# Performance work log

Measured on AMD Instinct MI355X. Metric: run time of the kernel, lower is better.

## Reference

```python
import jax, jax.numpy as jnp
import numpy as np

B, H, S, D = 2, 16, 1024, 64

def setup_inputs() -> dict:
    key = jax.random.key(0)
    k1, k2 = jax.random.split(key)
    # x1 is the output of a softmax (attention probabilities): non-negative, rows sum to 1
    logits = jax.random.normal(k1, (B, H, S, S), dtype=jnp.float32)
    x1 = jax.nn.softmax(logits, axis=-1)
    x2 = jax.random.normal(k2, (B, H, S, D), dtype=jnp.float32)
    return {"x1": x1, "x2": x2}

def reference(x1, x2):
    # Forward of EfficientMemoryGEMMWithSoftmax: exact batched GEMM.
    # (The outlier/low-bit compression only affects what is cached for backward;
    #  the forward output is the exact product.)
    return jnp.einsum('bhsk,bhkd->bhsd', x1, x2)
```

## Files before the change

kernel.cpp:

```cpp
#include <hip/hip_runtime.h>
#include <hip/hip_bf16.h>

typedef __attribute__((ext_vector_type(8))) short short8_t;
typedef __attribute__((ext_vector_type(4))) short short4_t;
typedef __attribute__((ext_vector_type(4))) float f32x4;

#define S_DIM   1024
#define D_DIM   64
#define BM      128
#define KC      64
#define NCHUNK  (S_DIM / KC)
#define BSTRIDE 72
#define THREADS 512

__device__ __forceinline__ ushort f2bf(float f) {
    __hip_bfloat16 h = __float2bfloat16(f);
    return __builtin_bit_cast(ushort, h);
}

__global__ __launch_bounds__(THREADS, 1)
void gemm_sm_kernel(const float* __restrict__ x1,
                    const float* __restrict__ x2,
                    float* __restrict__ out) {
    __shared__ ushort lds_a[BM * KC];
    __shared__ ushort lds_b[D_DIM * BSTRIDE];

    const int tid = threadIdx.x;
    const int bid = blockIdx.x;
    const int batch   = (bid & 7) * 4 + (bid >> 6);
    const int rowtile = (bid >> 3) & 7;
    const int row0    = rowtile * BM;

    const float* Abase = x1 + (size_t)batch * (S_DIM * S_DIM) + (size_t)row0 * S_DIM;
    const float* Bbase = x2 + (size_t)batch * (S_DIM * D_DIM);
    float*       Cbase = out + (size_t)batch * (S_DIM * D_DIM) + (size_t)row0 * D_DIM;

    const int w = tid >> 6;
    const int l = tid & 63;

    const int ar  = tid >> 2;
    const int akq = tid & 3;
    const float* aptr = Abase + (size_t)ar * S_DIM + akq * 16;
    const int aw_swz  = (ar & 7) << 3;
    const int aw_base = ar * KC + akq * 16;
    const int aw0 = (aw_base    ) ^ aw_swz;
    const int aw1 = (aw_base + 8) ^ aw_swz;

    const int bd  = l;
    const int bk0 = w * 4;

    const int wm = w >> 1, wn = w & 1;
    const int fr = l & 15, fg = l >> 4;
    int aidx[2][2], bidx[2][2];
    #pragma unroll
    for (int mf = 0; mf < 2; ++mf) {
        const int row = wm * 32 + mf * 16 + fr;
        #pragma unroll
        for (int ks = 0; ks < 2; ++ks)
            aidx[mf][ks] = (row * KC + ks * 32 + fg * 8) ^ ((row & 7) << 3);
    }
    #pragma unroll
    for (int nf = 0; nf < 2; ++nf) {
        const int col = wn * 32 + nf * 16 + fr;
        #pragma unroll
        for (int ks = 0; ks < 2; ++ks)
            bidx[nf][ks] = col * BSTRIDE + ks * 32 + fg * 8;
    }

    float areg[16];
    float breg[8];

    auto load_chunk = [&](int t) {
        const float* p = aptr + t * KC;
        #pragma unroll
        for (int i = 0; i < 4; ++i) {
            float4 v = *reinterpret_cast<const float4*>(p + i * 4);
            areg[i * 4 + 0] = v.x; areg[i * 4 + 1] = v.y;
            areg[i * 4 + 2] = v.z; areg[i * 4 + 3] = v.w;
        }
        const float* bp = Bbase + (size_t)t * KC * D_DIM + bd;
        #pragma unroll
        for (int i = 0; i < 2; ++i)
            #pragma unroll
            for (int j = 0; j < 4; ++j)
                breg[i * 4 + j] = bp[(bk0 + 32 * i + j) * D_DIM];
    };

    auto store_lds = [&]() {
        short8_t v0, v1;
        #pragma unroll
        for (int j = 0; j < 8; ++j) v0[j] = (short)f2bf(areg[j]);
        #pragma unroll
        for (int j = 0; j < 8; ++j) v1[j] = (short)f2bf(areg[8 + j]);
        *reinterpret_cast<short8_t*>(&lds_a[aw0]) = v0;
        *reinterpret_cast<short8_t*>(&lds_a[aw1]) = v1;
        #pragma unroll
        for (int i = 0; i < 2; ++i) {
            short4_t bv;
            #pragma unroll
            for (int j = 0; j < 4; ++j) bv[j] = (short)f2bf(breg[i * 4 + j]);
            *reinterpret_cast<short4_t*>(&lds_b[bd * BSTRIDE + bk0 + 32 * i]) = bv;
        }
    };

    f32x4 acc[2][2];
    #pragma unroll
    for (int mf = 0; mf < 2; ++mf)
        #pragma unroll
        for (int nf = 0; nf < 2; ++nf)
            acc[mf][nf] = f32x4{0.f, 0.f, 0.f, 0.f};

    load_chunk(0);

    for (int t = 0; t < NCHUNK; ++t) {
        __syncthreads();
        store_lds();
        __syncthreads();
        if (t + 1 < NCHUNK) load_chunk(t + 1);

        short8_t af[2][2], bf[2][2];
        #pragma unroll
        for (int mf = 0; mf < 2; ++mf)
            #pragma unroll
            for (int ks = 0; ks < 2; ++ks)
                af[mf][ks] = *reinterpret_cast<const short8_t*>(&lds_a[aidx[mf][ks]]);
        #pragma unroll
        for (int nf = 0; nf < 2; ++nf)
            #pragma unroll
            for (int ks = 0; ks < 2; ++ks)
                bf[nf][ks] = *reinterpret_cast<const short8_t*>(&lds_b[bidx[nf][ks]]);

        #pragma unroll
        for (int ks = 0; ks < 2; ++ks)
            #pragma unroll
            for (int mf = 0; mf < 2; ++mf)
                #pragma unroll
                for (int nf = 0; nf < 2; ++nf)
                    acc[mf][nf] = __builtin_amdgcn_mfma_f32_16x16x32_bf16(
                        af[mf][ks], bf[nf][ks], acc[mf][nf], 0, 0, 0);
    }

    #pragma unroll
    for (int mf = 0; mf < 2; ++mf)
        #pragma unroll
        for (int nf = 0; nf < 2; ++nf)
            #pragma unroll
            for (int j = 0; j < 4; ++j) {
                const int r = wm * 32 + mf * 16 + fg * 4 + j;
                const int c = wn * 32 + nf * 16 + fr;
                Cbase[(size_t)r * D_DIM + c] = acc[mf][nf][j];
            }
}

extern "C" void kernel_launch(void* const* d_in, const int* in_sizes, int n_in,
                              void* d_out, int out_size, void* d_ws, size_t ws_size,
                              hipStream_t stream) {
    const float* x1 = (const float*)d_in[0];
    const float* x2 = (const float*)d_in[1];
    float* out = (float*)d_out;
    dim3 grid(256), block(THREADS);
    gemm_sm_kernel<<<grid, block, 0, stream>>>(x1, x2, out);
}
```

Baseline: 32.39 us.

## Double-buffer LDS and register prefetch two chunks ahead with a single barrier

Measured after the change: 28.17 us. 1.15x faster.

```diff
diff --git a/kernel.cpp b/kernel.cpp
--- a/kernel.cpp
+++ b/kernel.cpp
@@ -18,12 +18,19 @@
     return __builtin_bit_cast(ushort, h);
 }
 
+#define SYNC() do { \
+    __builtin_amdgcn_sched_barrier(0); \
+    asm volatile("s_waitcnt lgkmcnt(0)"); \
+    __builtin_amdgcn_s_barrier(); \
+    __builtin_amdgcn_sched_barrier(0); \
+} while (0)
+
 __global__ __launch_bounds__(THREADS, 1)
 void gemm_sm_kernel(const float* __restrict__ x1,
                     const float* __restrict__ x2,
                     float* __restrict__ out) {
-    __shared__ ushort lds_a[BM * KC];
-    __shared__ ushort lds_b[D_DIM * BSTRIDE];
+    __shared__ ushort lds_a[2][BM * KC];
+    __shared__ ushort lds_b[2][D_DIM * BSTRIDE];
 
     const int tid = threadIdx.x;
     const int bid = blockIdx.x;
@@ -67,39 +74,39 @@
             bidx[nf][ks] = col * BSTRIDE + ks * 32 + fg * 8;
     }
 
-    float areg[16];
-    float breg[8];
+    float a0[16], a1[16], b0[8], b1[8];
 
-    auto load_chunk = [&](int t) {
+    auto load_chunk = [&](int t, float (&A)[16], float (&B)[8]) {
         const float* p = aptr + t * KC;
         #pragma unroll
         for (int i = 0; i < 4; ++i) {
             float4 v = *reinterpret_cast<const float4*>(p + i * 4);
-            areg[i * 4 + 0] = v.x; areg[i * 4 + 1] = v.y;
-            areg[i * 4 + 2] = v.z; areg[i * 4 + 3] = v.w;
+            A[i * 4 + 0] = v.x; A[i * 4 + 1] = v.y;
+            A[i * 4 + 2] = v.z; A[i * 4 + 3] = v.w;
         }
         const float* bp = Bbase + (size_t)t * KC * D_DIM + bd;
         #pragma unroll
         for (int i = 0; i < 2; ++i)
             #pragma unroll
             for (int j = 0; j < 4; ++j)
-                breg[i * 4 + j] = bp[(bk0 + 32 * i + j) * D_DIM];
+                B[i * 4 + j] = bp[(bk0 + 32 * i + j) * D_DIM];
     };
 
-    auto store_lds = [&]() {
+    auto store_chunk = [&](ushort* la, ushort* lb,
+                           const float (&A)[16], const float (&B)[8]) {
         short8_t v0, v1;
         #pragma unroll
-        for (int j = 0; j < 8; ++j) v0[j] = (short)f2bf(areg[j]);
+        for (int j = 0; j < 8; ++j) v0[j] = (short)f2bf(A[j]);
         #pragma unroll
-        for (int j = 0; j < 8; ++j) v1[j] = (short)f2bf(areg[8 + j]);
-        *reinterpret_cast<short8_t*>(&lds_a[aw0]) = v0;
-        *reinterpret_cast<short8_t*>(&lds_a[aw1]) = v1;
+        for (int j = 0; j < 8; ++j) v1[j] = (short)f2bf(A[8 + j]);
+        *reinterpret_cast<short8_t*>(&la[aw0]) = v0;
+        *reinterpret_cast<short8_t*>(&la[aw1]) = v1;
         #pragma unroll
         for (int i = 0; i < 2; ++i) {
             short4_t bv;
             #pragma unroll
-            for (int j = 0; j < 4; ++j) bv[j] = (short)f2bf(breg[i * 4 + j]);
-            *reinterpret_cast<short4_t*>(&lds_b[bd * BSTRIDE + bk0 + 32 * i]) = bv;
+            for (int j = 0; j < 4; ++j) bv[j] = (short)f2bf(B[i * 4 + j]);
+            *reinterpret_cast<short4_t*>(&lb[bd * BSTRIDE + bk0 + 32 * i]) = bv;
         }
     };
 
@@ -110,26 +117,18 @@
         for (int nf = 0; nf < 2; ++nf)
             acc[mf][nf] = f32x4{0.f, 0.f, 0.f, 0.f};
 
-    load_chunk(0);
-
-    for (int t = 0; t < NCHUNK; ++t) {
-        __syncthreads();
-        store_lds();
-        __syncthreads();
-        if (t + 1 < NCHUNK) load_chunk(t + 1);
-
+    auto compute = [&](const ushort* la, const ushort* lb) {
         short8_t af[2][2], bf[2][2];
         #pragma unroll
         for (int mf = 0; mf < 2; ++mf)
             #pragma unroll
             for (int ks = 0; ks < 2; ++ks)
-                af[mf][ks] = *reinterpret_cast<const short8_t*>(&lds_a[aidx[mf][ks]]);
+                af[mf][ks] = *reinterpret_cast<const short8_t*>(&la[aidx[mf][ks]]);
         #pragma unroll
         for (int nf = 0; nf < 2; ++nf)
             #pragma unroll
             for (int ks = 0; ks < 2; ++ks)
-                bf[nf][ks] = *reinterpret_cast<const short8_t*>(&lds_b[bidx[nf][ks]]);
-
+                bf[nf][ks] = *reinterpret_cast<const short8_t*>(&lb[bidx[nf][ks]]);
         #pragma unroll
         for (int ks = 0; ks < 2; ++ks)
             #pragma unroll
@@ -138,6 +137,24 @@
                 for (int nf = 0; nf < 2; ++nf)
                     acc[mf][nf] = __builtin_amdgcn_mfma_f32_16x16x32_bf16(
                         af[mf][ks], bf[nf][ks], acc[mf][nf], 0, 0, 0);
+    };
+
+    load_chunk(0, a0, b0);
+    load_chunk(1, a1, b1);
+    store_chunk(&lds_a[0][0], &lds_b[0][0], a0, b0);
+    SYNC();
+
+    #pragma unroll 1
+    for (int ti = 0; ti < NCHUNK; ti += 2) {
+        if (ti + 2 < NCHUNK) load_chunk(ti + 2, a0, b0);
+        store_chunk(&lds_a[1][0], &lds_b[1][0], a1, b1);
+        compute(&lds_a[0][0], &lds_b[0][0]);
+        SYNC();
+
+        if (ti + 3 < NCHUNK) load_chunk(ti + 3, a1, b1);
+        if (ti + 2 < NCHUNK) store_chunk(&lds_a[0][0], &lds_b[0][0], a0, b0);
+        compute(&lds_a[1][0], &lds_b[1][0]);
+        SYNC();
     }
 
     #pragma unroll
```
